# Optimization experiments

Hardware: AMD Instinct MI355X
Metric: run time of the kernel (lower is better)

Reference implementation:

```python
import jax, jax.numpy as jnp
import numpy as np

HEADS = 16
DIM_HEAD = 64
QUERY_DIM = 1024
INNER = HEADS * DIM_HEAD
SCALE = DIM_HEAD ** -0.5


def setup_inputs() -> dict:
    key = jax.random.key(0)
    ks = jax.random.split(key, 6)
    B, N, M = 2, 2048, 2048
    x = jax.random.normal(ks[0], (B, N, QUERY_DIM), dtype=jnp.float32)
    context = jax.random.normal(ks[1], (B, M, QUERY_DIM), dtype=jnp.float32)
    s = QUERY_DIM ** -0.5
    # weights stored [in, out] so y = x @ W matches torch Linear(x) with W = weight.T
    Wq = jax.random.normal(ks[2], (QUERY_DIM, INNER), dtype=jnp.float32) * s
    Wk = jax.random.normal(ks[3], (QUERY_DIM, INNER), dtype=jnp.float32) * s
    Wv = jax.random.normal(ks[4], (QUERY_DIM, INNER), dtype=jnp.float32) * s
    Wo = jax.random.normal(ks[5], (INNER, QUERY_DIM), dtype=jnp.float32) * (INNER ** -0.5)
    return {"x": x, "context": context, "Wq": Wq, "Wk": Wk, "Wv": Wv, "Wo": Wo}


def reference(x, context, Wq, Wk, Wv, Wo):
    B, N, _ = x.shape
    M = context.shape[1]
    # projections -> [b, n, h, d]
    q = (x @ Wq).reshape(B, N, HEADS, DIM_HEAD)
    k = (context @ Wk).reshape(B, M, HEADS, DIM_HEAD)
    v = (context @ Wv).reshape(B, M, HEADS, DIM_HEAD)
    sim = jnp.einsum('bihd,bjhd->bhij', q, k) * SCALE  # [b, h, n, m]
    attn = jax.nn.softmax(sim, axis=-1)
    out = jnp.einsum('bhij,bjhd->bihd', attn, v)  # [b, n, h, d]
    out = out.reshape(B, N, INNER)
    return out @ Wo
```

## Files before the change

kernel.cpp:

```cpp
#include <hip/hip_runtime.h>
#include <hip/hip_bf16.h>


typedef __attribute__((ext_vector_type(8))) __bf16    bf16x8;
typedef __attribute__((ext_vector_type(4))) __bf16    bf16x4;
typedef __attribute__((ext_vector_type(4))) float     f32x4;

#define B_    2
#define H_    16
#define N_    2048
#define M_    2048
#define D_    64
#define QD_   1024

#define QSCALE 0.18033688011112042f

__device__ __forceinline__ void gld16(const __bf16* g, __bf16* l) {
    __builtin_amdgcn_global_load_lds(
        (const __attribute__((address_space(1))) unsigned int*)(g),
        (__attribute__((address_space(3))) unsigned int*)(l), 16, 0, 0);
}

__global__ __launch_bounds__(256) void cvt2_f32_bf16(const float* __restrict__ x,
                                                     const float* __restrict__ ctx,
                                                     __bf16* __restrict__ xb,
                                                     __bf16* __restrict__ cb) {
    const float* src = blockIdx.y ? ctx : x;
    __bf16*      dst = blockIdx.y ? cb  : xb;
    int i = (blockIdx.x * 256 + threadIdx.x) * 4;
    float4 v = *reinterpret_cast<const float4*>(src + i);
    bf16x4 o;
    o.x = (__bf16)v.x; o.y = (__bf16)v.y; o.z = (__bf16)v.z; o.w = (__bf16)v.w;
    *reinterpret_cast<bf16x4*>(dst + i) = o;
}

__global__ __launch_bounds__(256) void transpose4_cvt(const float* __restrict__ w0,
                                                      const float* __restrict__ w1,
                                                      const float* __restrict__ w2,
                                                      const float* __restrict__ w3,
                                                      __bf16* __restrict__ t0,
                                                      __bf16* __restrict__ t1,
                                                      __bf16* __restrict__ t2,
                                                      __bf16* __restrict__ t3) {
    __shared__ float tile[64][65];
    const int z = blockIdx.z;
    const float* in = (z == 0) ? w0 : (z == 1) ? w1 : (z == 2) ? w2 : w3;
    __bf16*     out = (z == 0) ? t0 : (z == 1) ? t1 : (z == 2) ? t2 : t3;
    const int i0 = blockIdx.x * 64;
    const int o0 = blockIdx.y * 64;
    const int t  = threadIdx.x;
    const int r  = t >> 4;
    const int c4 = (t & 15) * 4;
#pragma unroll
    for (int p = 0; p < 4; ++p) {
        int row = p * 16 + r;
        float4 v = *reinterpret_cast<const float4*>(in + (size_t)(i0 + row) * QD_ + o0 + c4);
        tile[row][c4 + 0] = v.x; tile[row][c4 + 1] = v.y;
        tile[row][c4 + 2] = v.z; tile[row][c4 + 3] = v.w;
    }
    __syncthreads();
#pragma unroll
    for (int p = 0; p < 4; ++p) {
        int orow = p * 16 + r;
        bf16x4 o;
        o.x = (__bf16)tile[c4 + 0][orow];
        o.y = (__bf16)tile[c4 + 1][orow];
        o.z = (__bf16)tile[c4 + 2][orow];
        o.w = (__bf16)tile[c4 + 3][orow];
        *reinterpret_cast<bf16x4*>(out + (size_t)(o0 + orow) * QD_ + i0 + c4) = o;
    }
}

#define GEMM_BODY(A_, Bt_)                                                                     \
    __shared__ __align__(16) __bf16 Alds[2][128 * 32];                                         \
    __shared__ __align__(16) __bf16 Blds[2][128 * 32];                                         \
    const int tid  = threadIdx.x;                                                              \
    const int wid  = tid >> 6;                                                                 \
    const int lane = tid & 63;                                                                 \
    const int l15  = lane & 15;                                                                \
    const int lg   = lane >> 4;                                                                \
    const int wr   = wid >> 1;                                                                 \
    const int wc   = wid & 1;                                                                  \
    const int rowBase = blockIdx.x * 128;                                                      \
    const int colBase = blockIdx.y * 128;                                                      \
    const int srow = wid * 32 + (lane >> 2);                                                   \
    const int sg   = ((lane & 3) ^ ((srow >> 1) & 3)) * 8;       \
    const __bf16* Ag  = A_  + (size_t)(rowBase + srow) * QD_ + sg;                             \
    const __bf16* Ag2 = Ag  + (size_t)16 * QD_;           \
    const __bf16* Bg  = Bt_ + (size_t)(colBase + srow) * QD_ + sg;                             \
    const __bf16* Bg2 = Bg  + (size_t)16 * QD_;                                                \
    const int sOff  = (wid * 32) * 32;                                                         \
    const int sOff2 = sOff + 16 * 32;                                                          \
    int aoff[4], boff[4];                                                                      \
    _Pragma("unroll")                                                                          \
    for (int m = 0; m < 4; ++m) {                                                              \
        int ra = wr * 64 + m * 16 + l15;                                                       \
        int rb = wc * 64 + m * 16 + l15;                                                       \
        aoff[m] = ra * 32 + ((lg ^ ((ra >> 1) & 3)) * 8);                                      \
        boff[m] = rb * 32 + ((lg ^ ((rb >> 1) & 3)) * 8);                                      \
    }                                                                                          \
    f32x4 acc[4][4] = {};                                                                      \
    gld16(Ag,  &Alds[0][sOff]);                                                                \
    gld16(Ag2, &Alds[0][sOff2]);                                                               \
    gld16(Bg,  &Blds[0][sOff]);                                                                \
    gld16(Bg2, &Blds[0][sOff2]);                                                               \
    __syncthreads();                                                                           \
    for (int t = 0; t < 32; t += 2) {                                                          \
        if (t + 1 < 32) {                                                                      \
            int kn = (t + 1) * 32;                                                             \
            gld16(Ag + kn,  &Alds[1][sOff]);                                                   \
            gld16(Ag2 + kn, &Alds[1][sOff2]);                                                  \
            gld16(Bg + kn,  &Blds[1][sOff]);                                                   \
            gld16(Bg2 + kn, &Blds[1][sOff2]);                                                  \
        }                                                                                      \
        GCOMPUTE(0)                                                                            \
        __syncthreads();                                                                       \
        if (t + 2 < 32) {                                                                      \
            int kn = (t + 2) * 32;                                                             \
            gld16(Ag + kn,  &Alds[0][sOff]);                                                   \
            gld16(Ag2 + kn, &Alds[0][sOff2]);                                                  \
            gld16(Bg + kn,  &Blds[0][sOff]);                                                   \
            gld16(Bg2 + kn, &Blds[0][sOff2]);                                                  \
        }                                                                                      \
        GCOMPUTE(1)                                                                            \
        __syncthreads();                                                                       \
    }

#define GCOMPUTE(BUF)                                                                          \
    {                                                                                          \
        bf16x8 a[4], b[4];                                                                     \
        _Pragma("unroll")                                                                      \
        for (int m = 0; m < 4; ++m)                                                            \
            a[m] = *reinterpret_cast<const bf16x8*>(&Alds[BUF][aoff[m]]);                      \
        _Pragma("unroll")                                                                      \
        for (int n = 0; n < 4; ++n)                                                            \
            b[n] = *reinterpret_cast<const bf16x8*>(&Blds[BUF][boff[n]]);                      \
        _Pragma("unroll")                                                                      \
        for (int m = 0; m < 4; ++m)                                                            \
            _Pragma("unroll")                                                                  \
            for (int n = 0; n < 4; ++n)                                                        \
                acc[m][n] = __builtin_amdgcn_mfma_f32_16x16x32_bf16(a[m], b[n], acc[m][n], 0, 0, 0); \
    }

__global__ __launch_bounds__(256) void gemm_qkv(const __bf16* __restrict__ xb,
                                                const __bf16* __restrict__ cb,
                                                const __bf16* __restrict__ Wtq,
                                                const __bf16* __restrict__ Wtk,
                                                const __bf16* __restrict__ Wtv,
                                                __bf16* __restrict__ Qb,
                                                __bf16* __restrict__ Kb,
                                                __bf16* __restrict__ Vt) {
    const int z = blockIdx.z;
    const __bf16* Asel = (z == 0) ? xb : cb;
    const __bf16* Bsel = (z == 0) ? Wtq : (z == 1) ? Wtk : Wtv;
    GEMM_BODY(Asel, Bsel)
#pragma unroll
    for (int m = 0; m < 4; ++m)
#pragma unroll
        for (int n = 0; n < 4; ++n)
#pragma unroll
            for (int r = 0; r < 4; ++r) {
                int rr = rowBase + wr * 64 + m * 16 + lg * 4 + r;
                int cc = colBase + wc * 64 + n * 16 + l15;
                float v = acc[m][n][r];
                int b_ = rr >> 11, nn = rr & 2047, hh = cc >> 6, dd = cc & 63;
                if (z == 0) {
                    Qb[((size_t)(b_ * H_ + hh) * N_ + nn) * D_ + dd] = (__bf16)(v * QSCALE);
                } else if (z == 1) {
                    Kb[((size_t)(b_ * H_ + hh) * N_ + nn) * D_ + dd] = (__bf16)v;
                } else {
                    Vt[((size_t)(b_ * H_ + hh) * D_ + dd) * M_ + nn] = (__bf16)v;
                }
            }
}

__global__ __launch_bounds__(256) void gemm_out(const __bf16* __restrict__ AO,
                                                const __bf16* __restrict__ Wto,
                                                float* __restrict__ out) {
    GEMM_BODY(AO, Wto)
#pragma unroll
    for (int m = 0; m < 4; ++m)
#pragma unroll
        for (int n = 0; n < 4; ++n)
#pragma unroll
            for (int r = 0; r < 4; ++r) {
                int rr = rowBase + wr * 64 + m * 16 + lg * 4 + r;
                int cc = colBase + wc * 64 + n * 16 + l15;
                out[(size_t)rr * QD_ + cc] = acc[m][n][r];
            }
}

__global__ __launch_bounds__(512, 4) void attn_kernel(const __bf16* __restrict__ Q,
                                                      const __bf16* __restrict__ K,
                                                      const __bf16* __restrict__ Vt,
                                                      __bf16* __restrict__ AO) {
    __shared__ __align__(16) __bf16 Klds[2][4096];
    __shared__ __align__(16) __bf16 Vlds[2][4096];

    const int logical = (blockIdx.x & 7) * 64 + (blockIdx.x >> 3);
    const int qt   = logical & 15;
    const int bh   = logical >> 4;
    const int b    = bh >> 4;
    const int h    = bh & 15;
    const int wid  = threadIdx.x >> 6;
    const int lane = threadIdx.x & 63;
    const int l15  = lane & 15;
    const int lg   = lane >> 4;
    const int qbase = qt * 128 + wid * 16;

    const __bf16* Qp = Q  + ((size_t)bh * N_ + qbase) * D_;
    const __bf16* Kp = K  + (size_t)bh * M_ * D_;
    const __bf16* Vp = Vt + (size_t)bh * D_ * M_;

    const int rg   = lane >> 3;
    const int ch   = lane & 7;
    const int skw  = (rg & 3) | ((wid & 1) << 2);
    const int kc   = (ch ^ skw) << 3;
    const int vc   = (ch ^ rg) << 3;
    const int srow = wid * 8 + rg;
    const int ldst = wid * 512;

#define STAGE(BUF, KV0)                                                        \
    gld16(Kp + (size_t)((KV0) + srow) * D_ + kc, &Klds[BUF][ldst]);            \
    gld16(Vp + (size_t)srow * M_ + (KV0) + vc,  &Vlds[BUF][ldst]);

    const int rm0 = ((l15 >> 2) * 8) + (l15 & 3);
    const int sq  = (l15 & 7) << 3;
    const int ak00 = rm0 * 64 + (( 0 + lg * 8) ^ sq);
    const int ak01 = rm0 * 64 + ((32 + lg * 8) ^ sq);
    const int ak10 = ak00 + 256;
    const int ak11 = ak01 + 256;
    const int av0 = l15 * 64 + (( 0 + lg * 8) ^ sq);
    const int av1 = l15 * 64 + ((32 + lg * 8) ^ sq);

    bf16x8 qf0 = *reinterpret_cast<const bf16x8*>(Qp + (size_t)l15 * D_ +      lg * 8);
    bf16x8 qf1 = *reinterpret_cast<const bf16x8*>(Qp + (size_t)l15 * D_ + 32 + lg * 8);

    bf16x8 onesf;
#pragma unroll
    for (int j = 0; j < 8; ++j) onesf[j] = (__bf16)1.0f;

    f32x4 o0 = {}, o1 = {}, o2 = {}, o3 = {}, ors = {};

#define COMPUTE(KB, VB, KOFF, AV)                                                               \
    {                                                                                           \
        bf16x8 k00 = *reinterpret_cast<const bf16x8*>((KB) + ak00 + (KOFF));                    \
        bf16x8 k01 = *reinterpret_cast<const bf16x8*>((KB) + ak01 + (KOFF));                    \
        bf16x8 k10 = *reinterpret_cast<const bf16x8*>((KB) + ak10 + (KOFF));                    \
        bf16x8 k11 = *reinterpret_cast<const bf16x8*>((KB) + ak11 + (KOFF));                    \
        bf16x8 v0  = *reinterpret_cast<const bf16x8*>((VB) + (AV));                             \
        bf16x8 v1  = *reinterpret_cast<const bf16x8*>((VB) + (AV) + 1024);                      \
        bf16x8 v2  = *reinterpret_cast<const bf16x8*>((VB) + (AV) + 2048);                      \
        bf16x8 v3  = *reinterpret_cast<const bf16x8*>((VB) + (AV) + 3072);                      \
        f32x4 s0 = {}, s1 = {};                                                                 \
        s0 = __builtin_amdgcn_mfma_f32_16x16x32_bf16(k00, qf0, s0, 0, 0, 0);                    \
        s0 = __builtin_amdgcn_mfma_f32_16x16x32_bf16(k01, qf1, s0, 0, 0, 0);                    \
        s1 = __builtin_amdgcn_mfma_f32_16x16x32_bf16(k10, qf0, s1, 0, 0, 0);                    \
        s1 = __builtin_amdgcn_mfma_f32_16x16x32_bf16(k11, qf1, s1, 0, 0, 0);                    \
        bf16x8 pf;                                                                              \
        pf[0] = (__bf16)__builtin_amdgcn_exp2f(s0[0]);                                          \
        pf[1] = (__bf16)__builtin_amdgcn_exp2f(s0[1]);                                          \
        pf[2] = (__bf16)__builtin_amdgcn_exp2f(s0[2]);                                          \
        pf[3] = (__bf16)__builtin_amdgcn_exp2f(s0[3]);                                          \
        pf[4] = (__bf16)__builtin_amdgcn_exp2f(s1[0]);                                          \
        pf[5] = (__bf16)__builtin_amdgcn_exp2f(s1[1]);                                          \
        pf[6] = (__bf16)__builtin_amdgcn_exp2f(s1[2]);                                          \
        pf[7] = (__bf16)__builtin_amdgcn_exp2f(s1[3]);                                          \
        ors = __builtin_amdgcn_mfma_f32_16x16x32_bf16(pf, onesf, ors, 0, 0, 0);                 \
        o0 = __builtin_amdgcn_mfma_f32_16x16x32_bf16(pf, v0, o0, 0, 0, 0);                      \
        o1 = __builtin_amdgcn_mfma_f32_16x16x32_bf16(pf, v1, o1, 0, 0, 0);                      \
        o2 = __builtin_amdgcn_mfma_f32_16x16x32_bf16(pf, v2, o2, 0, 0, 0);                      \
        o3 = __builtin_amdgcn_mfma_f32_16x16x32_bf16(pf, v3, o3, 0, 0, 0);                      \
    }

    STAGE(0, 0)
    __syncthreads();

    for (int t = 0; t < 32; t += 2) {
        if (t + 1 < 32) { STAGE(1, (t + 1) * 64) }
        COMPUTE(Klds[0], Vlds[0], 0,    av0)
        COMPUTE(Klds[0], Vlds[0], 2048, av1)
        __syncthreads();
        if (t + 2 < 32) { STAGE(0, (t + 2) * 64) }
        COMPUTE(Klds[1], Vlds[1], 0,    av0)
        COMPUTE(Klds[1], Vlds[1], 2048, av1)
        __syncthreads();
    }
#undef STAGE
#undef COMPUTE

#pragma unroll
    for (int r = 0; r < 4; ++r) {
        float inv = 1.0f / ors[r];
        size_t row = ((size_t)b * N_ + qbase + lg * 4 + r) * QD_ + h * D_ + l15;
        AO[row +  0] = (__bf16)(o0[r] * inv);
        AO[row + 16] = (__bf16)(o1[r] * inv);
        AO[row + 32] = (__bf16)(o2[r] * inv);
        AO[row + 48] = (__bf16)(o3[r] * inv);
    }
}

extern "C" void kernel_launch(void* const* d_in, const int* in_sizes, int n_in,
                              void* d_out, int out_size, void* d_ws, size_t ws_size,
                              hipStream_t stream) {
    const float* x   = (const float*)d_in[0];
    const float* ctx = (const float*)d_in[1];
    const float* Wq  = (const float*)d_in[2];
    const float* Wk  = (const float*)d_in[3];
    const float* Wv  = (const float*)d_in[4];
    const float* Wo  = (const float*)d_in[5];

    char* ws = (char*)d_ws;
    __bf16* xb  = (__bf16*)(ws);
    __bf16* cb  = (__bf16*)(ws + (8u  << 20));
    __bf16* Wtq = (__bf16*)(ws + (16u << 20));
    __bf16* Wtk = (__bf16*)(ws + (18u << 20));
    __bf16* Wtv = (__bf16*)(ws + (20u << 20));
    __bf16* Wto = (__bf16*)(ws + (22u << 20));
    __bf16* Qb  = (__bf16*)(ws + (24u << 20));
    __bf16* Kb  = (__bf16*)(ws + (32u << 20));
    __bf16* Vt  = (__bf16*)(ws + (40u << 20));
    __bf16* AO  = (__bf16*)(ws + (48u << 20));

    cvt2_f32_bf16<<<dim3(4096, 2), 256, 0, stream>>>(x, ctx, xb, cb);
    transpose4_cvt<<<dim3(16, 16, 4), 256, 0, stream>>>(Wq, Wk, Wv, Wo, Wtq, Wtk, Wtv, Wto);
    gemm_qkv<<<dim3(32, 8, 3), 256, 0, stream>>>(xb, cb, Wtq, Wtk, Wtv, Qb, Kb, Vt);
    attn_kernel<<<512, 512, 0, stream>>>(Qb, Kb, Vt, AO);
    gemm_out<<<dim3(32, 8), 256, 0, stream>>>(AO, Wto, (float*)d_out);
}
```

Before: 122.8 us.

## Triple-buffer GEMM LDS tiles with prefetch distance two and partial vmcnt waits

```diff
diff --git a/kernel.cpp b/kernel.cpp
--- a/kernel.cpp
+++ b/kernel.cpp
@@ -72,8 +72,8 @@
 }
 
 #define GEMM_BODY(A_, Bt_)                                                                     \
-    __shared__ __align__(16) __bf16 Alds[2][128 * 32];                                         \
-    __shared__ __align__(16) __bf16 Blds[2][128 * 32];                                         \
+    __shared__ __align__(16) __bf16 Alds[3][128 * 32];                                         \
+    __shared__ __align__(16) __bf16 Blds[3][128 * 32];                                         \
     const int tid  = threadIdx.x;                                                              \
     const int wid  = tid >> 6;                                                                 \
     const int lane = tid & 63;                                                                 \
@@ -86,7 +86,7 @@
     const int srow = wid * 32 + (lane >> 2);                                                   \
     const int sg   = ((lane & 3) ^ ((srow >> 1) & 3)) * 8;       \
     const __bf16* Ag  = A_  + (size_t)(rowBase + srow) * QD_ + sg;                             \
-    const __bf16* Ag2 = Ag  + (size_t)16 * QD_;           \
+    const __bf16* Ag2 = Ag  + (size_t)16 * QD_;                                                \
     const __bf16* Bg  = Bt_ + (size_t)(colBase + srow) * QD_ + sg;                             \
     const __bf16* Bg2 = Bg  + (size_t)16 * QD_;                                                \
     const int sOff  = (wid * 32) * 32;                                                         \
@@ -100,30 +100,30 @@
         boff[m] = rb * 32 + ((lg ^ ((rb >> 1) & 3)) * 8);                                      \
     }                                                                                          \
     f32x4 acc[4][4] = {};                                                                      \
-    gld16(Ag,  &Alds[0][sOff]);                                                                \
-    gld16(Ag2, &Alds[0][sOff2]);                                                               \
-    gld16(Bg,  &Blds[0][sOff]);                                                                \
-    gld16(Bg2, &Blds[0][sOff2]);                                                               \
-    __syncthreads();                                                                           \
-    for (int t = 0; t < 32; t += 2) {                                                          \
-        if (t + 1 < 32) {                                                                      \
-            int kn = (t + 1) * 32;                                                             \
-            gld16(Ag + kn,  &Alds[1][sOff]);                                                   \
-            gld16(Ag2 + kn, &Alds[1][sOff2]);                                                  \
-            gld16(Bg + kn,  &Blds[1][sOff]);                                                   \
-            gld16(Bg2 + kn, &Blds[1][sOff2]);                                                  \
-        }                                                                                      \
-        GCOMPUTE(0)                                                                            \
-        __syncthreads();                                                                       \
+                                                            \
+    gld16(Ag,            &Alds[0][sOff]);                                                      \
+    gld16(Ag2,           &Alds[0][sOff2]);                                                     \
+    gld16(Bg,            &Blds[0][sOff]);                                                      \
+    gld16(Bg2,           &Blds[0][sOff2]);                                                     \
+    gld16(Ag  + 32,      &Alds[1][sOff]);                                                      \
+    gld16(Ag2 + 32,      &Alds[1][sOff2]);                                                     \
+    gld16(Bg  + 32,      &Blds[1][sOff]);                                                      \
+    gld16(Bg2 + 32,      &Blds[1][sOff2]);                                                     \
+    int cur = 0, nxt2 = 2;                                                                     \
+    for (int t = 0; t < 32; ++t) {                                                             \
+        if (t != 31) { asm volatile("s_waitcnt vmcnt(4)" ::: "memory"); }                      \
+        else         { asm volatile("s_waitcnt vmcnt(0)" ::: "memory"); }                      \
+        __builtin_amdgcn_s_barrier();                                                          \
         if (t + 2 < 32) {                                                                      \
             int kn = (t + 2) * 32;                                                             \
-            gld16(Ag + kn,  &Alds[0][sOff]);                                                   \
-            gld16(Ag2 + kn, &Alds[0][sOff2]);                                                  \
-            gld16(Bg + kn,  &Blds[0][sOff]);                                                   \
-            gld16(Bg2 + kn, &Blds[0][sOff2]);                                                  \
+            gld16(Ag  + kn, &Alds[nxt2][sOff]);                                                \
+            gld16(Ag2 + kn, &Alds[nxt2][sOff2]);                                               \
+            gld16(Bg  + kn, &Blds[nxt2][sOff]);                                                \
+            gld16(Bg2 + kn, &Blds[nxt2][sOff2]);                                               \
         }                                                                                      \
-        GCOMPUTE(1)                                                                            \
-        __syncthreads();                                                                       \
+        GCOMPUTE(cur)                                                                          \
+        cur = (cur == 2) ? 0 : cur + 1;                                                        \
+        nxt2 = (nxt2 == 2) ? 0 : nxt2 + 1;                                                     \
     }
 
 #define GCOMPUTE(BUF)                                                                          \
```

Result: slower. 126.6 us (+3.1%).

## Merge prep kernels into one launch and shrink GEMM tiles to 128x64

Applied to the files above, without the earlier changes.

```diff
diff --git a/kernel.cpp b/kernel.cpp
--- a/kernel.cpp
+++ b/kernel.cpp
@@ -21,31 +21,37 @@
         (__attribute__((address_space(3))) unsigned int*)(l), 16, 0, 0);
 }
 
-__global__ __launch_bounds__(256) void cvt2_f32_bf16(const float* __restrict__ x,
-                                                     const float* __restrict__ ctx,
-                                                     __bf16* __restrict__ xb,
-                                                     __bf16* __restrict__ cb) {
-    const float* src = blockIdx.y ? ctx : x;
-    __bf16*      dst = blockIdx.y ? cb  : xb;
-    int i = (blockIdx.x * 256 + threadIdx.x) * 4;
-    float4 v = *reinterpret_cast<const float4*>(src + i);
-    bf16x4 o;
-    o.x = (__bf16)v.x; o.y = (__bf16)v.y; o.z = (__bf16)v.z; o.w = (__bf16)v.w;
-    *reinterpret_cast<bf16x4*>(dst + i) = o;
-}
-
-__global__ __launch_bounds__(256) void transpose4_cvt(const float* __restrict__ w0,
-                                                      const float* __restrict__ w1,
-                                                      const float* __restrict__ w2,
-                                                      const float* __restrict__ w3,
-                                                      __bf16* __restrict__ t0,
-                                                      __bf16* __restrict__ t1,
-                                                      __bf16* __restrict__ t2,
-                                                      __bf16* __restrict__ t3) {
+__global__ __launch_bounds__(256) void prep(const float* __restrict__ x,
+                                            const float* __restrict__ ctx,
+                                            const float* __restrict__ w0,
+                                            const float* __restrict__ w1,
+                                            const float* __restrict__ w2,
+                                            const float* __restrict__ w3,
+                                            __bf16* __restrict__ xb,
+                                            __bf16* __restrict__ cb,
+                                            __bf16* __restrict__ t0,
+                                            __bf16* __restrict__ t1,
+                                            __bf16* __restrict__ t2,
+                                            __bf16* __restrict__ t3) {
     __shared__ float tile[64][65];
     const int z = blockIdx.z;
-    const float* in = (z == 0) ? w0 : (z == 1) ? w1 : (z == 2) ? w2 : w3;
-    __bf16*     out = (z == 0) ? t0 : (z == 1) ? t1 : (z == 2) ? t2 : t3;
+    if (z < 2) {
+        const float* src = z ? ctx : x;
+        __bf16*      dst = z ? cb  : xb;
+        const size_t base = (size_t)(blockIdx.y * 16 + blockIdx.x) * 16384;
+#pragma unroll
+        for (int p = 0; p < 16; ++p) {
+            size_t i = base + p * 1024 + threadIdx.x * 4;
+            float4 v = *reinterpret_cast<const float4*>(src + i);
+            bf16x4 o;
+            o.x = (__bf16)v.x; o.y = (__bf16)v.y; o.z = (__bf16)v.z; o.w = (__bf16)v.w;
+            *reinterpret_cast<bf16x4*>(dst + i) = o;
+        }
+        return;
+    }
+    const int w = z - 2;
+    const float* in = (w == 0) ? w0 : (w == 1) ? w1 : (w == 2) ? w2 : w3;
+    __bf16*     out = (w == 0) ? t0 : (w == 1) ? t1 : (w == 2) ? t2 : t3;
     const int i0 = blockIdx.x * 64;
     const int o0 = blockIdx.y * 64;
     const int t  = threadIdx.x;
@@ -73,7 +79,7 @@
 
 #define GEMM_BODY(A_, Bt_)                                                                     \
     __shared__ __align__(16) __bf16 Alds[2][128 * 32];                                         \
-    __shared__ __align__(16) __bf16 Blds[2][128 * 32];                                         \
+    __shared__ __align__(16) __bf16 Blds[2][64 * 32];                                          \
     const int tid  = threadIdx.x;                                                              \
     const int wid  = tid >> 6;                                                                 \
     const int lane = tid & 63;                                                                 \
@@ -82,45 +88,47 @@
     const int wr   = wid >> 1;                                                                 \
     const int wc   = wid & 1;                                                                  \
     const int rowBase = blockIdx.x * 128;                                                      \
-    const int colBase = blockIdx.y * 128;                                                      \
-    const int srow = wid * 32 + (lane >> 2);                                                   \
-    const int sg   = ((lane & 3) ^ ((srow >> 1) & 3)) * 8;       \
-    const __bf16* Ag  = A_  + (size_t)(rowBase + srow) * QD_ + sg;                             \
-    const __bf16* Ag2 = Ag  + (size_t)16 * QD_;           \
-    const __bf16* Bg  = Bt_ + (size_t)(colBase + srow) * QD_ + sg;                             \
-    const __bf16* Bg2 = Bg  + (size_t)16 * QD_;                                                \
-    const int sOff  = (wid * 32) * 32;                                                         \
-    const int sOff2 = sOff + 16 * 32;                                                          \
-    int aoff[4], boff[4];                                                                      \
+    const int colBase = blockIdx.y * 64;                                                       \
+    const int srowA = wid * 32 + (lane >> 2);                                                  \
+    const int srowB = wid * 16 + (lane >> 2);                                                  \
+    const int sgA   = ((lane & 3) ^ ((srowA >> 1) & 3)) * 8;                                   \
+    const int sgB   = ((lane & 3) ^ ((srowB >> 1) & 3)) * 8;                                   \
+    const __bf16* Ag  = A_  + (size_t)(rowBase + srowA) * QD_ + sgA;                           \
+    const __bf16* Ag2 = Ag  + (size_t)16 * QD_;        \
+    const __bf16* Bg  = Bt_ + (size_t)(colBase + srowB) * QD_ + sgB;                           \
+    const int sOffA  = (wid * 32) * 32;                                                        \
+    const int sOffA2 = sOffA + 16 * 32;                                                        \
+    const int sOffB  = (wid * 16) * 32;                                                        \
+    int aoff[4], boff[2];                                                                      \
     _Pragma("unroll")                                                                          \
     for (int m = 0; m < 4; ++m) {                                                              \
         int ra = wr * 64 + m * 16 + l15;                                                       \
-        int rb = wc * 64 + m * 16 + l15;                                                       \
         aoff[m] = ra * 32 + ((lg ^ ((ra >> 1) & 3)) * 8);                                      \
-        boff[m] = rb * 32 + ((lg ^ ((rb >> 1) & 3)) * 8);                                      \
     }                                                                                          \
-    f32x4 acc[4][4] = {};                                                                      \
-    gld16(Ag,  &Alds[0][sOff]);                                                                \
-    gld16(Ag2, &Alds[0][sOff2]);                                                               \
-    gld16(Bg,  &Blds[0][sOff]);                                                                \
-    gld16(Bg2, &Blds[0][sOff2]);                                                               \
+    _Pragma("unroll")                                                                          \
+    for (int n = 0; n < 2; ++n) {                                                              \
+        int rb = wc * 32 + n * 16 + l15;                                                       \
+        boff[n] = rb * 32 + ((lg ^ ((rb >> 1) & 3)) * 8);                                      \
+    }                                                                                          \
+    f32x4 acc[4][2] = {};                                                                      \
+    gld16(Ag,  &Alds[0][sOffA]);                                                               \
+    gld16(Ag2, &Alds[0][sOffA2]);                                                              \
+    gld16(Bg,  &Blds[0][sOffB]);                                                               \
     __syncthreads();                                                                           \
     for (int t = 0; t < 32; t += 2) {                                                          \
         if (t + 1 < 32) {                                                                      \
             int kn = (t + 1) * 32;                                                             \
-            gld16(Ag + kn,  &Alds[1][sOff]);                                                   \
-            gld16(Ag2 + kn, &Alds[1][sOff2]);                                                  \
-            gld16(Bg + kn,  &Blds[1][sOff]);                                                   \
-            gld16(Bg2 + kn, &Blds[1][sOff2]);                                                  \
+            gld16(Ag + kn,  &Alds[1][sOffA]);                                                  \
+            gld16(Ag2 + kn, &Alds[1][sOffA2]);                                                 \
+            gld16(Bg + kn,  &Blds[1][sOffB]);                                                  \
         }                                                                                      \
         GCOMPUTE(0)                                                                            \
         __syncthreads();                                                                       \
         if (t + 2 < 32) {                                                                      \
             int kn = (t + 2) * 32;                                                             \
-            gld16(Ag + kn,  &Alds[0][sOff]);                                                   \
-            gld16(Ag2 + kn, &Alds[0][sOff2]);                                                  \
-            gld16(Bg + kn,  &Blds[0][sOff]);                                                   \
-            gld16(Bg2 + kn, &Blds[0][sOff2]);                                                  \
+            gld16(Ag + kn,  &Alds[0][sOffA]);                                                  \
+            gld16(Ag2 + kn, &Alds[0][sOffA2]);                                                 \
+            gld16(Bg + kn,  &Blds[0][sOffB]);                                                  \
         }                                                                                      \
         GCOMPUTE(1)                                                                            \
         __syncthreads();                                                                       \
@@ -128,17 +136,17 @@
 
 #define GCOMPUTE(BUF)                                                                          \
     {                                                                                          \
-        bf16x8 a[4], b[4];                                                                     \
+        bf16x8 a[4], b[2];                                                                     \
         _Pragma("unroll")                                                                      \
         for (int m = 0; m < 4; ++m)                                                            \
             a[m] = *reinterpret_cast<const bf16x8*>(&Alds[BUF][aoff[m]]);                      \
         _Pragma("unroll")                                                                      \
-        for (int n = 0; n < 4; ++n)                                                            \
+        for (int n = 0; n < 2; ++n)                                                            \
             b[n] = *reinterpret_cast<const bf16x8*>(&Blds[BUF][boff[n]]);                      \
         _Pragma("unroll")                                                                      \
         for (int m = 0; m < 4; ++m)                                                            \
             _Pragma("unroll")                                                                  \
-            for (int n = 0; n < 4; ++n)                                                        \
+            for (int n = 0; n < 2; ++n)                                                        \
                 acc[m][n] = __builtin_amdgcn_mfma_f32_16x16x32_bf16(a[m], b[n], acc[m][n], 0, 0, 0); \
     }
 
@@ -157,11 +165,11 @@
 #pragma unroll
     for (int m = 0; m < 4; ++m)
 #pragma unroll
-        for (int n = 0; n < 4; ++n)
+        for (int n = 0; n < 2; ++n)
 #pragma unroll
             for (int r = 0; r < 4; ++r) {
                 int rr = rowBase + wr * 64 + m * 16 + lg * 4 + r;
-                int cc = colBase + wc * 64 + n * 16 + l15;
+                int cc = colBase + wc * 32 + n * 16 + l15;
                 float v = acc[m][n][r];
                 int b_ = rr >> 11, nn = rr & 2047, hh = cc >> 6, dd = cc & 63;
                 if (z == 0) {
@@ -181,11 +189,11 @@
 #pragma unroll
     for (int m = 0; m < 4; ++m)
 #pragma unroll
-        for (int n = 0; n < 4; ++n)
+        for (int n = 0; n < 2; ++n)
 #pragma unroll
             for (int r = 0; r < 4; ++r) {
                 int rr = rowBase + wr * 64 + m * 16 + lg * 4 + r;
-                int cc = colBase + wc * 64 + n * 16 + l15;
+                int cc = colBase + wc * 32 + n * 16 + l15;
                 out[(size_t)rr * QD_ + cc] = acc[m][n][r];
             }
 }
@@ -322,9 +330,9 @@
     __bf16* Vt  = (__bf16*)(ws + (40u << 20));
     __bf16* AO  = (__bf16*)(ws + (48u << 20));
 
-    cvt2_f32_bf16<<<dim3(4096, 2), 256, 0, stream>>>(x, ctx, xb, cb);
-    transpose4_cvt<<<dim3(16, 16, 4), 256, 0, stream>>>(Wq, Wk, Wv, Wo, Wtq, Wtk, Wtv, Wto);
-    gemm_qkv<<<dim3(32, 8, 3), 256, 0, stream>>>(xb, cb, Wtq, Wtk, Wtv, Qb, Kb, Vt);
+    prep<<<dim3(16, 16, 6), 256, 0, stream>>>(x, ctx, Wq, Wk, Wv, Wo,
+                                              xb, cb, Wtq, Wtk, Wtv, Wto);
+    gemm_qkv<<<dim3(32, 16, 3), 256, 0, stream>>>(xb, cb, Wtq, Wtk, Wtv, Qb, Kb, Vt);
     attn_kernel<<<512, 512, 0, stream>>>(Qb, Kb, Vt, AO);
-    gemm_out<<<dim3(32, 8), 256, 0, stream>>>(AO, Wto, (float*)d_out);
-}
+    gemm_out<<<dim3(32, 16), 256, 0, stream>>>(AO, Wto, (float*)d_out);
+}
```

After: 124.6 us. About the same (+1.5%).
